# Kernel optimization log

Measured on AMD Instinct MI355X. Metric: run time of the kernel, lower is better.

## Reference

```python
import jax, jax.numpy as jnp
import numpy as np

NNODE = 6000
NELEM = 12000
NFIX = 200
NDLOAD = 400


def create_Dmat(nu, E):
    c = E / ((1.0 + nu) * (1.0 - 2.0 * nu))
    return c * jnp.array([[1.0 - nu, nu, 0.0],
                          [nu, 1.0 - nu, 0.0],
                          [0.0, 0.0, (1.0 - 2.0 * nu) / 2.0]], dtype=jnp.float32)


def setup_inputs() -> dict:
    key = jax.random.key(0)
    ks = jax.random.split(key, 10)
    xcoord = jax.random.uniform(ks[0], (NNODE,), dtype=jnp.float32) * 100.0
    ycoord = jax.random.uniform(ks[1], (NNODE,), dtype=jnp.float32) * 100.0
    # build connectivity with guaranteed-distinct node triples (avoids zero-area elements)
    r = jax.random.randint(ks[2], (NELEM,), 0, NNODE)
    connect = jnp.stack([r, (r + 1) % NNODE, (r + 2) % NNODE], axis=1).astype(jnp.int32)
    elem_material = jax.random.uniform(ks[3], (NELEM,), dtype=jnp.float32)
    dload_elem = jax.random.randint(ks[4], (NDLOAD,), 0, NELEM, dtype=jnp.int32)
    dload_face = jax.random.randint(ks[5], (NDLOAD,), 0, 3, dtype=jnp.int32)
    dload_tx = jax.random.normal(ks[6], (NDLOAD,), dtype=jnp.float32)
    dload_ty = jax.random.normal(ks[7], (NDLOAD,), dtype=jnp.float32)
    fix_node = jax.random.randint(ks[8], (NFIX,), 0, NNODE, dtype=jnp.int32)
    fix_dof = jax.random.randint(ks[9], (NFIX,), 0, 2, dtype=jnp.int32)
    fix_val = jax.random.normal(jax.random.fold_in(key, 99), (NFIX,), dtype=jnp.float32)
    return {"xcoord": xcoord, "ycoord": ycoord, "connect": connect,
            "elem_material": elem_material, "dload_elem": dload_elem,
            "dload_face": dload_face, "dload_tx": dload_tx, "dload_ty": dload_ty,
            "fix_node": fix_node, "fix_dof": fix_dof, "fix_val": fix_val}


def _assemble(xcoord, ycoord, connect, elem_material,
              dload_elem, dload_face, dload_tx, dload_ty,
              fix_node, fix_dof, fix_val):
    nnode = xcoord.shape[0]
    ndof = 2 * nnode
    Dmat_st = create_Dmat(0.3, 200.0)   # steel
    Dmat_al = create_Dmat(0.33, 69.0)   # aluminium

    # gather element node coordinates: [nelem]
    xa, xb, xc = (xcoord[connect[:, i]] for i in range(3))
    ya, yb, yc = (ycoord[connect[:, i]] for i in range(3))

    den_a = (ya - yb) * (xc - xb) - (xa - xb) * (yc - yb)
    den_b = (yb - yc) * (xa - xc) - (xb - xc) * (ya - yc)
    den_c = (yc - ya) * (xb - xa) - (xc - xa) * (yb - ya)
    nax = -(yc - yb) / den_a
    nay = (xc - xb) / den_a
    nbx = -(ya - yc) / den_b
    nby = (xa - xc) / den_b
    ncx = -(yb - ya) / den_c
    ncy = (xb - xa) / den_c
    area = 0.5 * jnp.abs((xb - xa) * (yc - ya) - (xc - xa) * (yb - ya))

    zero = jnp.zeros_like(nax)
    # Bmat per element: [nelem, 3, 6]
    B = jnp.stack([
        jnp.stack([nax, zero, nbx, zero, ncx, zero], axis=-1),
        jnp.stack([zero, nay, zero, nby, zero, ncy], axis=-1),
        jnp.stack([nay, nax, nby, nbx, ncy, ncx], axis=-1),
    ], axis=1)

    # per-element material matrix: [nelem, 3, 3]
    D = jnp.where(elem_material[:, None, None] > 0.5, Dmat_al, Dmat_st)

    # element stiffness k = area * B^T D B : [nelem, 6, 6]
    k = jnp.einsum('eki,ekl,elj->eij', B, D, B) * area[:, None, None]

    # DOF indices per element, ordered [2a,2a+1,2b,2b+1,2c,2c+1]
    dofs = jnp.stack([2 * connect, 2 * connect + 1], axis=-1).reshape(-1, 6)

    stiff = jnp.zeros((ndof, ndof), dtype=jnp.float32)
    stiff = stiff.at[dofs[:, :, None], dofs[:, None, :]].add(k)

    # distributed (traction) loads on element faces
    pointer = jnp.array([1, 2, 0], dtype=jnp.int32)
    a = connect[dload_elem, dload_face]
    b = connect[dload_elem, pointer[dload_face]]
    dx = xcoord[a] - xcoord[b]
    dy = ycoord[a] - ycoord[b]
    half_len = 0.5 * jnp.sqrt(dx * dx + dy * dy)
    rdofs = jnp.stack([2 * a, 2 * a + 1, 2 * b, 2 * b + 1], axis=-1)   # [d,4]
    rvals = jnp.stack([dload_tx, dload_ty, dload_tx, dload_ty], axis=-1) * half_len[:, None]
    resid = jnp.zeros((ndof,), dtype=jnp.float32).at[rdofs].add(rvals)

    # essential BCs: zero row, unit diagonal, prescribed value
    rw = 2 * fix_node + fix_dof
    row_mask = jnp.zeros((ndof,), dtype=jnp.float32).at[rw].set(1.0)
    stiff = stiff * (1.0 - row_mask)[:, None]
    stiff = stiff.at[rw, rw].set(1.0)
    resid = resid.at[rw].set(fix_val)

    return stiff, resid[:, None]


def reference(xcoord, ycoord, connect, elem_material, dload_elem, dload_face,
              dload_tx, dload_ty, fix_node, fix_dof, fix_val):
    return _assemble(xcoord, ycoord, connect, elem_material,
                     dload_elem, dload_face, dload_tx, dload_ty,
                     fix_node, fix_dof, fix_val)
```

## Files before the change

### kernel.cpp

```cpp
#include <hip/hip_runtime.h>


#define ADJ_CAP 64


__global__ void build_adj_kernel(const int* __restrict__ connect, int nelem,
                                 const int* __restrict__ fix_node,
                                 const int* __restrict__ fix_dof, int nfix,
                                 int* __restrict__ cnt,
                                 int* __restrict__ mask,
                                 int* __restrict__ adj) {
    int t = blockIdx.x * blockDim.x + threadIdx.x;
    if (t < nelem) {
#pragma unroll
        for (int v = 0; v < 3; ++v) {
            int n = connect[3 * t + v];
            int slot = atomicAdd(&cnt[n], 1);
            if (slot < ADJ_CAP) adj[n * ADJ_CAP + slot] = (t << 2) | v;
        }
    }
    if (t < nfix) {
        mask[2 * fix_node[t] + fix_dof[t]] = 1;
    }
}

__global__ __launch_bounds__(256) void row_write_kernel(
        const float* __restrict__ x, const float* __restrict__ y,
        const int* __restrict__ connect, const float* __restrict__ mat,
        const int* __restrict__ cnt, const int* __restrict__ mask,
        const int* __restrict__ adj,
        float* __restrict__ stiff, int ndof) {
    extern __shared__ float row[];
    const int r = blockIdx.x;
    const int tid = threadIdx.x;
    const int n = r >> 1;
    const int d = r & 1;

    float4* row4 = (float4*)row;
    const int n4 = ndof >> 2;
    for (int i = tid; i < n4; i += 256) row4[i] = make_float4(0.f, 0.f, 0.f, 0.f);
    __syncthreads();

    const bool is_fixed = (mask[r] != 0);
    if (is_fixed) {
        if (tid == 0) row[r] = 1.0f;
    } else {
        int deg = cnt[n];
        if (deg > ADJ_CAP) deg = ADJ_CAP;
        if (tid < deg) {
            const int packed = adj[n * ADJ_CAP + tid];
            const int e  = packed >> 2;
            const int li = packed & 3;

            const int a = connect[3 * e + 0];
            const int b = connect[3 * e + 1];
            const int c = connect[3 * e + 2];
            const float xa = x[a], xb = x[b], xc = x[c];
            const float ya = y[a], yb = y[b], yc = y[c];

            const float den_a = (ya - yb) * (xc - xb) - (xa - xb) * (yc - yb);
            const float den_b = (yb - yc) * (xa - xc) - (xb - xc) * (ya - yc);
            const float den_c = (yc - ya) * (xb - xa) - (xc - xa) * (yb - ya);

            const float nax = -(yc - yb) / den_a;
            const float nay =  (xc - xb) / den_a;
            const float nbx = -(ya - yc) / den_b;
            const float nby =  (xa - xc) / den_b;
            const float ncx = -(yb - ya) / den_c;
            const float ncy =  (xb - xa) / den_c;

            const float area = 0.5f * fabsf((xb - xa) * (yc - ya) -
                                            (xc - xa) * (yb - ya));

            float nu, E;
            if (mat[e] > 0.5f) { nu = 0.33f; E = 69.0f; }
            else               { nu = 0.30f; E = 200.0f; }
            const float cc  = E / ((1.0f + nu) * (1.0f - 2.0f * nu));
            const float d00 = cc * (1.0f - nu);
            const float d01 = cc * nu;
            const float d22 = cc * (1.0f - 2.0f * nu) * 0.5f;

            const float B0[6] = { nax, 0.f, nbx, 0.f, ncx, 0.f };
            const float B1[6] = { 0.f, nay, 0.f, nby, 0.f, ncy };
            const float B2[6] = { nay, nax, nby, nbx, ncy, ncx };

            const float nx = (li == 0) ? nax : (li == 1) ? nbx : ncx;
            const float ny = (li == 0) ? nay : (li == 1) ? nby : ncy;
            const float Bi0 = (d == 0) ? nx : 0.f;
            const float Bi1 = (d == 0) ? 0.f : ny;
            const float Bi2 = (d == 0) ? ny : nx;

            const int dof[6] = { 2 * a, 2 * a + 1, 2 * b, 2 * b + 1,
                                 2 * c, 2 * c + 1 };
#pragma unroll
            for (int j = 0; j < 6; ++j) {
                const float C0j = d00 * B0[j] + d01 * B1[j];
                const float C1j = d01 * B0[j] + d00 * B1[j];
                const float C2j = d22 * B2[j];
                const float val = area * (Bi0 * C0j + Bi1 * C1j + Bi2 * C2j);
                atomicAdd(&row[dof[j]], val);
            }
        }
    }
    __syncthreads();

    float4* dst = (float4*)(stiff + (size_t)r * (size_t)ndof);
    for (int i = tid; i < n4; i += 256) dst[i] = row4[i];
}

__global__ void traction_kernel(const float* __restrict__ x,
                                const float* __restrict__ y,
                                const int* __restrict__ connect,
                                const int* __restrict__ dload_elem,
                                const int* __restrict__ dload_face,
                                const float* __restrict__ tx,
                                const float* __restrict__ ty,
                                float* __restrict__ resid,
                                int ndload) {
    int i = blockIdx.x * blockDim.x + threadIdx.x;
    if (i >= ndload) return;
    int e = dload_elem[i];
    int f = dload_face[i];
    int f2 = (f == 0) ? 1 : (f == 1 ? 2 : 0);
    int a = connect[3 * e + f];
    int b = connect[3 * e + f2];
    float dx = x[a] - x[b];
    float dy = y[a] - y[b];
    float hl = 0.5f * sqrtf(dx * dx + dy * dy);
    float vx = tx[i] * hl;
    float vy = ty[i] * hl;
    atomicAdd(&resid[2 * a + 0], vx);
    atomicAdd(&resid[2 * a + 1], vy);
    atomicAdd(&resid[2 * b + 0], vx);
    atomicAdd(&resid[2 * b + 1], vy);
}

__global__ void fix_resid_kernel(const int* __restrict__ fix_node,
                                 const int* __restrict__ fix_dof,
                                 const float* __restrict__ fix_val,
                                 float* __restrict__ resid, int nfix) {
    int i = blockIdx.x * blockDim.x + threadIdx.x;
    if (i >= nfix) return;
    int rw = 2 * fix_node[i] + fix_dof[i];
    bool last = true;
    for (int j = i + 1; j < nfix; ++j) {
        if (2 * fix_node[j] + fix_dof[j] == rw) { last = false; break; }
    }
    if (last) resid[rw] = fix_val[i];
}

extern "C" void kernel_launch(void* const* d_in, const int* in_sizes, int n_in,
                              void* d_out, int out_size, void* d_ws, size_t ws_size,
                              hipStream_t stream) {
    const float* xcoord   = (const float*)d_in[0];
    const float* ycoord   = (const float*)d_in[1];
    const int*   connect  = (const int*)d_in[2];
    const float* emat     = (const float*)d_in[3];
    const int*   dl_elem  = (const int*)d_in[4];
    const int*   dl_face  = (const int*)d_in[5];
    const float* dl_tx    = (const float*)d_in[6];
    const float* dl_ty    = (const float*)d_in[7];
    const int*   fix_node = (const int*)d_in[8];
    const int*   fix_dof  = (const int*)d_in[9];
    const float* fix_val  = (const float*)d_in[10];

    const int nnode  = in_sizes[0];
    const int ndof   = 2 * nnode;
    const int nelem  = in_sizes[3];
    const int ndload = in_sizes[4];
    const int nfix   = in_sizes[8];

    float* stiff = (float*)d_out;
    float* resid = stiff + (size_t)ndof * (size_t)ndof;

    int* cnt  = (int*)d_ws;
    int* mask = cnt + nnode;
    int* adj  = mask + ndof;

    hipMemsetAsync(d_ws, 0, (size_t)(nnode + ndof) * sizeof(int), stream);
    hipMemsetAsync(resid, 0, (size_t)ndof * sizeof(float), stream);

    {
        int threads = 256;
        int blocks = (nelem + threads - 1) / threads;
        build_adj_kernel<<<blocks, threads, 0, stream>>>(
            connect, nelem, fix_node, fix_dof, nfix, cnt, mask, adj);
    }

    row_write_kernel<<<ndof, 256, (size_t)ndof * sizeof(float), stream>>>(
        xcoord, ycoord, connect, emat, cnt, mask, adj, stiff, ndof);

    {
        int threads = 256;
        int blocks = (ndload + threads - 1) / threads;
        traction_kernel<<<blocks, threads, 0, stream>>>(
            xcoord, ycoord, connect, dl_elem, dl_face, dl_tx, dl_ty,
            resid, ndload);
    }
    {
        int threads = 256;
        int blocks = (nfix + threads - 1) / threads;
        fix_resid_kernel<<<blocks, threads, 0, stream>>>(
            fix_node, fix_dof, fix_val, resid, nfix);
    }
}
```

Measured before the change: 150.2 us.

## Replace dense shared-memory row with sparse list plus bitmap and streaming stores

Each row block no longer zeroes and atomically accumulates into a full ndof-sized shared-memory row. Instead, each element contribution is appended to a small shared list, and a bitmap marks which columns are non-zero. During the write-out, each float4 chunk checks the bitmap: chunks with no marked columns store zeros directly, and marked chunks are summed from the list. Stores are now nontemporal. Dropping the roughly 48KB of dynamic LDS per block should raise occupancy for this write-bandwidth-bound kernel. The cost is a hardcoded 512-word bitmap (at most 16384 dofs) and a capped list that could silently drop contributions on very high-degree nodes.

```diff
diff --git a/kernel.cpp b/kernel.cpp
--- a/kernel.cpp
+++ b/kernel.cpp
@@ -1,7 +1,10 @@
 #include <hip/hip_runtime.h>
 
 
-#define ADJ_CAP 64
+#define ADJ_CAP  64
+#define LIST_CAP 256
+
+typedef float fx4 __attribute__((ext_vector_type(4)));
 
 
 __global__ void build_adj_kernel(const int* __restrict__ connect, int nelem,
@@ -30,20 +33,26 @@
         const int* __restrict__ cnt, const int* __restrict__ mask,
         const int* __restrict__ adj,
         float* __restrict__ stiff, int ndof) {
-    extern __shared__ float row[];
-    const int r = blockIdx.x;
+    __shared__ unsigned int bitmap[512];
+    __shared__ int   lcols[LIST_CAP];
+    __shared__ float lvals[LIST_CAP];
+    __shared__ int   lcount;
+
+    const int r   = blockIdx.x;
     const int tid = threadIdx.x;
-    const int n = r >> 1;
-    const int d = r & 1;
-
-    float4* row4 = (float4*)row;
-    const int n4 = ndof >> 2;
-    for (int i = tid; i < n4; i += 256) row4[i] = make_float4(0.f, 0.f, 0.f, 0.f);
+    const int n   = r >> 1;
+    const int d   = r & 1;
+    const int nwords = (ndof + 31) >> 5;
+
+    for (int i = tid; i < nwords; i += 256) bitmap[i] = 0u;
+    if (tid == 0) lcount = 0;
     __syncthreads();
 
-    const bool is_fixed = (mask[r] != 0);
-    if (is_fixed) {
-        if (tid == 0) row[r] = 1.0f;
+    if (mask[r] != 0) {
+        if (tid == 0) {
+            lcols[0] = r; lvals[0] = 1.0f; lcount = 1;
+            atomicOr(&bitmap[r >> 5], 1u << (r & 31));
+        }
     } else {
         int deg = cnt[n];
         if (deg > ADJ_CAP) deg = ADJ_CAP;
@@ -98,14 +107,39 @@
                 const float C1j = d01 * B0[j] + d00 * B1[j];
                 const float C2j = d22 * B2[j];
                 const float val = area * (Bi0 * C0j + Bi1 * C1j + Bi2 * C2j);
-                atomicAdd(&row[dof[j]], val);
+                const int   col = dof[j];
+                int slot = atomicAdd(&lcount, 1);
+                if (slot < LIST_CAP) {
+                    lcols[slot] = col;
+                    lvals[slot] = val;
+                    atomicOr(&bitmap[col >> 5], 1u << (col & 31));
+                }
             }
         }
     }
     __syncthreads();
 
-    float4* dst = (float4*)(stiff + (size_t)r * (size_t)ndof);
-    for (int i = tid; i < n4; i += 256) dst[i] = row4[i];
+    const int nlist = (lcount < LIST_CAP) ? lcount : LIST_CAP;
+    fx4* dst4 = (fx4*)(stiff + (size_t)r * (size_t)ndof);
+    const int n4 = ndof >> 2;
+    for (int i = tid; i < n4; i += 256) {
+        const int c0 = i << 2;
+        const unsigned int bits = (bitmap[c0 >> 5] >> (c0 & 31)) & 0xFu;
+        fx4 v = (fx4){0.f, 0.f, 0.f, 0.f};
+        if (bits) {
+            float v0 = 0.f, v1 = 0.f, v2 = 0.f, v3 = 0.f;
+            for (int k = 0; k < nlist; ++k) {
+                const int   col = lcols[k];
+                const float val = lvals[k];
+                v0 += (col == c0    ) ? val : 0.f;
+                v1 += (col == c0 + 1) ? val : 0.f;
+                v2 += (col == c0 + 2) ? val : 0.f;
+                v3 += (col == c0 + 3) ? val : 0.f;
+            }
+            v = (fx4){v0, v1, v2, v3};
+        }
+        __builtin_nontemporal_store(v, &dst4[i]);
+    }
 }
 
 __global__ void traction_kernel(const float* __restrict__ x,
@@ -177,8 +211,8 @@
     int* mask = cnt + nnode;
     int* adj  = mask + ndof;
 
-    hipMemsetAsync(d_ws, 0, (size_t)(nnode + ndof) * sizeof(int), stream);
-    hipMemsetAsync(resid, 0, (size_t)ndof * sizeof(float), stream);
+    (void)hipMemsetAsync(d_ws, 0, (size_t)(nnode + ndof) * sizeof(int), stream);
+    (void)hipMemsetAsync(resid, 0, (size_t)ndof * sizeof(float), stream);
 
     {
         int threads = 256;
@@ -187,7 +221,7 @@
             connect, nelem, fix_node, fix_dof, nfix, cnt, mask, adj);
     }
 
-    row_write_kernel<<<ndof, 256, (size_t)ndof * sizeof(float), stream>>>(
+    row_write_kernel<<<ndof, 256, 0, stream>>>(
         xcoord, ycoord, connect, emat, cnt, mask, adj, stiff, ndof);
 
     {
```

New measurement: 154.6 us. 3.0% more time.
